# Kernel optimization log

Hardware: AMD Instinct MI355X
Metric: run time of the kernel (lower is better)

The kernel has to match this reference:

```python
import jax, jax.numpy as jnp
import numpy as np

B, N, VDIM = 64, 256, 2048
LRDIM, EMBED = 64, 1024


def setup_inputs() -> dict:
    key = jax.random.key(0)
    ks = jax.random.split(key, 12)
    s = 1.0 / np.sqrt(VDIM)
    return {
        "Vmat": jax.random.normal(ks[0], (B, N, VDIM), dtype=jnp.float32),
        # weight-normed linear_U1: W = g * v / ||v||_row, bias b
        "U1_v": jax.random.normal(ks[1], (LRDIM, VDIM), dtype=jnp.float32) * s,
        "U1_g": jax.random.uniform(ks[2], (LRDIM,), dtype=jnp.float32, minval=0.5, maxval=1.5),
        "U1_b": jax.random.normal(ks[3], (LRDIM,), dtype=jnp.float32) * s,
        "U2_v": jax.random.normal(ks[4], (LRDIM, VDIM), dtype=jnp.float32) * s,
        "U2_g": jax.random.uniform(ks[5], (LRDIM,), dtype=jnp.float32, minval=0.5, maxval=1.5),
        "U2_b": jax.random.normal(ks[6], (LRDIM,), dtype=jnp.float32) * s,
        # final projection + BatchNorm1d affine params
        "W_lin": jax.random.normal(ks[7], (EMBED, VDIM), dtype=jnp.float32) * s,
        "b_lin": jax.random.normal(ks[8], (EMBED,), dtype=jnp.float32) * s,
        "bn_gamma": jnp.ones((EMBED,), dtype=jnp.float32),
        "bn_beta": jnp.zeros((EMBED,), dtype=jnp.float32),
    }


def _weight_norm(v, g):
    # torch weight_norm with dim=0: per output row
    return v * (g / jnp.linalg.norm(v, axis=1))[:, None]


def reference(Vmat, U1_v, U1_g, U1_b, U2_v, U2_g, U2_b, W_lin, b_lin, bn_gamma, bn_beta):
    # forward(Vmat, t_method='uncorr', model_num=6) -> UnCorrVmat_Detail path
    W1 = _weight_norm(U1_v, U1_g)
    W2 = _weight_norm(U2_v, U2_g)
    right = jax.nn.relu(jnp.einsum('bnv,kv->bnk', Vmat, W1) + U1_b)   # [B,N,LR]
    left = jax.nn.relu(jnp.einsum('bnv,kv->bnk', Vmat, W2) + U2_b)    # [B,N,LR]
    uncorr = jnp.einsum('bnk,bmk->bnm', left, right)                   # [B,N,N]
    # vectorized per-batch diag rsqrt normalization
    d = jax.lax.rsqrt(jnp.einsum('bii->bi', uncorr) + 1e-6)            # [B,N]
    uncorr = d[:, None, :] * uncorr * d[:, :, None]
    uncorr = 1.0 + jnp.eye(Vmat.shape[1], dtype=Vmat.dtype) - uncorr
    feats = jnp.mean(jnp.einsum('bnm,bmv->bnv', uncorr, Vmat), axis=1)  # [B,VDIM]
    # linear + BatchNorm1d (training mode: biased batch stats)
    x = feats @ W_lin.T + b_lin                                        # [B,EMBED]
    mu = jnp.mean(x, axis=0)
    var = jnp.mean(jnp.square(x - mu), axis=0)
    return bn_gamma * (x - mu) * jax.lax.rsqrt(var + 1e-5) + bn_beta
```

## Files before the change

kernel.cpp:

```cpp
#include <hip/hip_runtime.h>

#define B_ 64
#define N_ 256
#define V_ 2048
#define E_ 1024
#define MROWS 16384

typedef __bf16 bf16_t;
typedef bf16_t bf16x8 __attribute__((ext_vector_type(8)));
typedef float f32x4 __attribute__((ext_vector_type(4)));

#define OFF_S   0
#define OFF_LR  16384
#define OFF_FT  2113536
#define FTSZ    131072
#define OFF_WB  2637824

__device__ __forceinline__ void gload_lds16(const bf16_t* g, bf16_t* l) {
    __builtin_amdgcn_global_load_lds((const __attribute__((address_space(1))) void*)g,
                                     (__attribute__((address_space(3))) void*)l, 16, 0, 0);
}

__global__ void kprep(const float* __restrict__ U1v, const float* __restrict__ U1g,
                      const float* __restrict__ U2v, const float* __restrict__ U2g,
                      bf16_t* __restrict__ Wb) {
    __shared__ float red[256];
    __shared__ float sc;
    const int r = blockIdx.x;
    const float* v = (r < 64) ? (U1v + (size_t)r * V_) : (U2v + (size_t)(r - 64) * V_);
    float ss = 0.f;
    for (int i = threadIdx.x; i < V_; i += 256) { float x = v[i]; ss += x * x; }
    red[threadIdx.x] = ss;
    __syncthreads();
    for (int o = 128; o > 0; o >>= 1) {
        if (threadIdx.x < (unsigned)o) red[threadIdx.x] += red[threadIdx.x + o];
        __syncthreads();
    }
    if (threadIdx.x == 0) {
        float g = (r < 64) ? U1g[r] : U2g[r - 64];
        sc = g * rsqrtf(red[0]);
    }
    __syncthreads();
    const float s = sc;
    const int k = threadIdx.x * 8;
    float4 f0 = *(const float4*)(v + k);
    float4 f1 = *(const float4*)(v + k + 4);
    bf16x8 o;
    o[0] = (bf16_t)(f0.x * s); o[1] = (bf16_t)(f0.y * s);
    o[2] = (bf16_t)(f0.z * s); o[3] = (bf16_t)(f0.w * s);
    o[4] = (bf16_t)(f1.x * s); o[5] = (bf16_t)(f1.y * s);
    o[6] = (bf16_t)(f1.z * s); o[7] = (bf16_t)(f1.w * s);
    *(bf16x8*)(Wb + (size_t)r * V_ + k) = o;
}

#define BK 128
__global__ __launch_bounds__(256) void gemm_lr(
    const float* __restrict__ V, const bf16_t* __restrict__ Wb,
    const float* __restrict__ U1b, const float* __restrict__ U2b,
    float* __restrict__ LR) {
    __shared__ bf16_t As[32 * BK];
    __shared__ bf16_t Bs[128 * BK];
    const int t = threadIdx.x;
    const int m0 = blockIdx.x * 32;
    const int wv = t >> 6, lane = t & 63;
    const int lm = lane & 15, lq = lane >> 4;
    const int n0w = wv * 32;

    const int ar = t >> 3, au = t & 7;
    const float* aptr = V + (size_t)(m0 + ar) * V_ + au * 8;
    bf16_t* adst0 = &As[ar * BK + ((au ^ (ar & 15)) * 8)];
    bf16_t* adst1 = &As[ar * BK + (((au + 8) ^ (ar & 15)) * 8)];

    const int rloc = lane >> 4, cc = lane & 15;
    const int r15 = wv * 4 + rloc;
    const bf16_t* bgsrc = Wb + (size_t)r15 * V_ + (cc ^ r15) * 8;

    f32x4 acc[2][2];
#pragma unroll
    for (int i = 0; i < 2; ++i)
#pragma unroll
        for (int j = 0; j < 2; ++j) acc[i][j] = (f32x4){0.f, 0.f, 0.f, 0.f};

#pragma unroll
    for (int q = 0; q < 8; ++q)
        gload_lds16(bgsrc + (size_t)q * 16 * V_, &Bs[(q * 16 + wv * 4) * BK]);
    float4 ap0 = *(const float4*)(aptr);
    float4 ap1 = *(const float4*)(aptr + 4);
    float4 ap2 = *(const float4*)(aptr + 64);
    float4 ap3 = *(const float4*)(aptr + 68);

    for (int k0 = 0; k0 < V_; k0 += BK) {
        bf16x8 av0, av1;
        av0[0] = (bf16_t)ap0.x; av0[1] = (bf16_t)ap0.y; av0[2] = (bf16_t)ap0.z; av0[3] = (bf16_t)ap0.w;
        av0[4] = (bf16_t)ap1.x; av0[5] = (bf16_t)ap1.y; av0[6] = (bf16_t)ap1.z; av0[7] = (bf16_t)ap1.w;
        av1[0] = (bf16_t)ap2.x; av1[1] = (bf16_t)ap2.y; av1[2] = (bf16_t)ap2.z; av1[3] = (bf16_t)ap2.w;
        av1[4] = (bf16_t)ap3.x; av1[5] = (bf16_t)ap3.y; av1[6] = (bf16_t)ap3.z; av1[7] = (bf16_t)ap3.w;
        *(bf16x8*)adst0 = av0;
        *(bf16x8*)adst1 = av1;
        __syncthreads();

#pragma unroll
        for (int h = 0; h < 2; ++h) {
            bf16x8 af[2][2], bfr[2][2];
#pragma unroll
            for (int i = 0; i < 2; ++i)
#pragma unroll
                for (int kf = 0; kf < 2; ++kf)
                    af[i][kf] = *(bf16x8*)&As[(i * 16 + lm) * BK + ((((h * 2 + kf) * 4 + lq) ^ lm) * 8)];
#pragma unroll
            for (int j = 0; j < 2; ++j)
#pragma unroll
                for (int kf = 0; kf < 2; ++kf)
                    bfr[j][kf] = *(bf16x8*)&Bs[(n0w + j * 16 + lm) * BK + ((((h * 2 + kf) * 4 + lq) ^ lm) * 8)];
            if (h == 1 && k0 + BK < V_) {
                ap0 = *(const float4*)(aptr + k0 + BK);
                ap1 = *(const float4*)(aptr + k0 + BK + 4);
                ap2 = *(const float4*)(aptr + k0 + BK + 64);
                ap3 = *(const float4*)(aptr + k0 + BK + 68);
            }
#pragma unroll
            for (int i = 0; i < 2; ++i)
#pragma unroll
                for (int j = 0; j < 2; ++j) {
                    acc[i][j] = __builtin_amdgcn_mfma_f32_16x16x32_bf16(af[i][0], bfr[j][0], acc[i][j], 0, 0, 0);
                    acc[i][j] = __builtin_amdgcn_mfma_f32_16x16x32_bf16(af[i][1], bfr[j][1], acc[i][j], 0, 0, 0);
                }
        }
        __syncthreads();
        if (k0 + BK < V_) {
#pragma unroll
            for (int q = 0; q < 8; ++q)
                gload_lds16(bgsrc + (size_t)q * 16 * V_ + (k0 + BK), &Bs[(q * 16 + wv * 4) * BK]);
        }
    }
#pragma unroll
    for (int j = 0; j < 2; ++j) {
        const int n = n0w + j * 16 + lm;
        const float bi = (n < 64) ? U1b[n] : U2b[n - 64];
#pragma unroll
        for (int i = 0; i < 2; ++i)
#pragma unroll
            for (int r = 0; r < 4; ++r) {
                const int m = m0 + i * 16 + lq * 4 + r;
                LR[(size_t)m * 128 + n] = fmaxf(acc[i][j][r] + bi, 0.f);
            }
    }
}

__global__ __launch_bounds__(256) void kds(const float* __restrict__ LR, float* __restrict__ s) {
    __shared__ float dl[256];
    __shared__ float red[4][64];
    __shared__ float lbar[64];
    const int b = blockIdx.x, t = threadIdx.x;
    const float* Lb = LR + (size_t)b * N_ * 128;
    const float* row = Lb + (size_t)t * 128;
    float dd = 0.f;
#pragma unroll
    for (int k = 0; k < 64; k += 4) {
        float4 l = *(const float4*)(row + k);
        float4 r = *(const float4*)(row + 64 + k);
        dd += l.x * r.x + l.y * r.y + l.z * r.z + l.w * r.w;
    }
    const float dv = rsqrtf(dd + 1e-6f);
    dl[t] = dv;
    __syncthreads();
    const int k = t & 63, g = t >> 6;
    float acc = 0.f;
    for (int n = g; n < N_; n += 4)
        acc += dl[n] * Lb[(size_t)n * 128 + 64 + k];
    red[g][k] = acc;
    __syncthreads();
    if (t < 64) lbar[t] = red[0][t] + red[1][t] + red[2][t] + red[3][t];
    __syncthreads();
    float a2 = 0.f;
#pragma unroll 8
    for (int kk = 0; kk < 64; ++kk) a2 += lbar[kk] * row[kk];
    s[b * N_ + t] = ((float)(N_ + 1) - dv * a2) * (1.0f / (float)N_);
}

__global__ __launch_bounds__(256) void kfeats(const float* __restrict__ Vmat,
                                              const float* __restrict__ s,
                                              float* __restrict__ ftp) {
    const int b = blockIdx.x >> 3, vc = (blockIdx.x >> 2) & 1, mc = blockIdx.x & 3;
    __shared__ float sl[64];
    const int t = threadIdx.x;
    if (t < 64) sl[t] = s[b * N_ + mc * 64 + t];
    __syncthreads();
    const int v = vc * 1024 + t * 4;
    const float* base = Vmat + (size_t)b * N_ * V_ + (size_t)mc * 64 * V_ + v;
    float4 a = {0.f, 0.f, 0.f, 0.f};
    for (int m = 0; m < 64; m += 16) {
        float4 x[16];
#pragma unroll
        for (int u = 0; u < 16; ++u) x[u] = *(const float4*)(base + (size_t)(m + u) * V_);
#pragma unroll
        for (int u = 0; u < 16; ++u) {
            float sv = sl[m + u];
            a.x += sv * x[u].x; a.y += sv * x[u].y;
            a.z += sv * x[u].z; a.w += sv * x[u].w;
        }
    }
    float* dst = ftp + (size_t)mc * FTSZ;
    dst[(size_t)(v + 0) * 64 + b] = a.x;
    dst[(size_t)(v + 1) * 64 + b] = a.y;
    dst[(size_t)(v + 2) * 64 + b] = a.z;
    dst[(size_t)(v + 3) * 64 + b] = a.w;
}

__global__ __launch_bounds__(512) void klinbn(const float* __restrict__ ftp,
                                              const float* __restrict__ Wl,
                                              const float* __restrict__ gamma,
                                              const float* __restrict__ beta,
                                              float* __restrict__ out) {
    __shared__ float red[8][4][64];
    const int e0 = blockIdx.x * 4;
    const int t = threadIdx.x, b = t & 63, g = t >> 6;
    const float* w0 = Wl + (size_t)(e0 + 0) * V_ + g * 256;
    const float* w1 = Wl + (size_t)(e0 + 1) * V_ + g * 256;
    const float* w2 = Wl + (size_t)(e0 + 2) * V_ + g * 256;
    const float* w3 = Wl + (size_t)(e0 + 3) * V_ + g * 256;
    const float* f0 = ftp + 0 * FTSZ + (size_t)g * 256 * 64 + b;
    const float* f1 = ftp + 1 * FTSZ + (size_t)g * 256 * 64 + b;
    const float* f2 = ftp + 2 * FTSZ + (size_t)g * 256 * 64 + b;
    const float* f3 = ftp + 3 * FTSZ + (size_t)g * 256 * 64 + b;
    float a0 = 0.f, a1 = 0.f, a2 = 0.f, a3 = 0.f;
#pragma unroll 4
    for (int k = 0; k < 256; ++k) {
        const size_t o = (size_t)k * 64;
        float fv = (f0[o] + f1[o]) + (f2[o] + f3[o]);
        a0 += fv * w0[k]; a1 += fv * w1[k]; a2 += fv * w2[k]; a3 += fv * w3[k];
    }
    red[g][0][b] = a0; red[g][1][b] = a1; red[g][2][b] = a2; red[g][3][b] = a3;
    __syncthreads();
    if (t < 256) {
        const int e = t >> 6;
        float v = 0.f;
#pragma unroll
        for (int gg = 0; gg < 8; ++gg) v += red[gg][e][b];
        float sum = v;
#pragma unroll
        for (int o = 1; o < 64; o <<= 1) sum += __shfl_xor(sum, o, 64);
        float mu = sum * (1.f / 64.f);
        float dvv = v - mu;
        float q = dvv * dvv;
#pragma unroll
        for (int o = 1; o < 64; o <<= 1) q += __shfl_xor(q, o, 64);
        float inv = rsqrtf(q * (1.f / 64.f) + 1e-5f);
        red[0][e][b] = gamma[e0 + e] * dvv * inv + beta[e0 + e];
    }
    __syncthreads();
    if (t < 256) {
        const int b2 = t >> 2, j = t & 3;
        out[(size_t)b2 * E_ + e0 + j] = red[0][j][b2];
    }
}

extern "C" void kernel_launch(void* const* d_in, const int* in_sizes, int n_in,
                              void* d_out, int out_size, void* d_ws, size_t ws_size,
                              hipStream_t stream) {
    const float* Vmat = (const float*)d_in[0];
    const float* U1v  = (const float*)d_in[1];
    const float* U1g  = (const float*)d_in[2];
    const float* U1b  = (const float*)d_in[3];
    const float* U2v  = (const float*)d_in[4];
    const float* U2g  = (const float*)d_in[5];
    const float* U2b  = (const float*)d_in[6];
    const float* Wl   = (const float*)d_in[7];
    const float* gam  = (const float*)d_in[9];
    const float* bet  = (const float*)d_in[10];

    float*  ws     = (float*)d_ws;
    float*  s      = ws + OFF_S;
    float*  LR     = ws + OFF_LR;
    float*  ftp    = ws + OFF_FT;
    bf16_t* Wb     = (bf16_t*)(ws + OFF_WB);

    kprep  <<<128, 256, 0, stream>>>(U1v, U1g, U2v, U2g, Wb);
    gemm_lr<<<MROWS / 32, 256, 0, stream>>>(Vmat, Wb, U1b, U2b, LR);
    kds    <<<B_, 256, 0, stream>>>(LR, s);
    kfeats <<<B_ * 8, 256, 0, stream>>>(Vmat, s, ftp);
    klinbn <<<E_ / 4, 512, 0, stream>>>(ftp, Wl, gam, bet, (float*)d_out);
}
```

Baseline: 289.3 us.

## Double-buffer LDS tiles in low-rank GEMM to overlap loads with MFMA

Doubles the A and B shared-memory tiles in gemm_lr so the next K-slice of both V (fp32 to bf16 converted) and the bf16 weights is fetched into the alternate buffer while MFMAs run on the current one. This drops one of the two barriers per iteration and moves the weight global-to-LDS loads off the critical path. In exchange LDS use doubles to 80 KB per block, which may cut occupancy, and the A prefetch registers now stay live across the whole compute phase.

```diff
diff --git a/kernel.cpp b/kernel.cpp
--- a/kernel.cpp
+++ b/kernel.cpp
@@ -54,12 +54,14 @@
 }
 
 #define BK 128
+#define ASZ (32 * BK)
+#define BSZ (128 * BK)
 __global__ __launch_bounds__(256) void gemm_lr(
     const float* __restrict__ V, const bf16_t* __restrict__ Wb,
     const float* __restrict__ U1b, const float* __restrict__ U2b,
     float* __restrict__ LR) {
-    __shared__ bf16_t As[32 * BK];
-    __shared__ bf16_t Bs[128 * BK];
+    __shared__ bf16_t As[2 * ASZ];
+    __shared__ bf16_t Bs[2 * BSZ];
     const int t = threadIdx.x;
     const int m0 = blockIdx.x * 32;
     const int wv = t >> 6, lane = t & 63;
@@ -68,12 +70,13 @@
 
     const int ar = t >> 3, au = t & 7;
     const float* aptr = V + (size_t)(m0 + ar) * V_ + au * 8;
-    bf16_t* adst0 = &As[ar * BK + ((au ^ (ar & 15)) * 8)];
-    bf16_t* adst1 = &As[ar * BK + (((au + 8) ^ (ar & 15)) * 8)];
+    const int aoff0 = ar * BK + ((au ^ (ar & 15)) * 8);
+    const int aoff1 = ar * BK + (((au + 8) ^ (ar & 15)) * 8);
 
     const int rloc = lane >> 4, cc = lane & 15;
     const int r15 = wv * 4 + rloc;
     const bf16_t* bgsrc = Wb + (size_t)r15 * V_ + (cc ^ r15) * 8;
+    const int bofw = wv * 4 * BK;
 
     f32x4 acc[2][2];
 #pragma unroll
@@ -81,24 +84,39 @@
 #pragma unroll
         for (int j = 0; j < 2; ++j) acc[i][j] = (f32x4){0.f, 0.f, 0.f, 0.f};
 
-#pragma unroll
-    for (int q = 0; q < 8; ++q)
-        gload_lds16(bgsrc + (size_t)q * 16 * V_, &Bs[(q * 16 + wv * 4) * BK]);
     float4 ap0 = *(const float4*)(aptr);
     float4 ap1 = *(const float4*)(aptr + 4);
     float4 ap2 = *(const float4*)(aptr + 64);
     float4 ap3 = *(const float4*)(aptr + 68);
-
-    for (int k0 = 0; k0 < V_; k0 += BK) {
+#pragma unroll
+    for (int q = 0; q < 8; ++q)
+        gload_lds16(bgsrc + (size_t)q * 16 * V_, &Bs[bofw + q * 16 * BK]);
+    {
         bf16x8 av0, av1;
         av0[0] = (bf16_t)ap0.x; av0[1] = (bf16_t)ap0.y; av0[2] = (bf16_t)ap0.z; av0[3] = (bf16_t)ap0.w;
         av0[4] = (bf16_t)ap1.x; av0[5] = (bf16_t)ap1.y; av0[6] = (bf16_t)ap1.z; av0[7] = (bf16_t)ap1.w;
         av1[0] = (bf16_t)ap2.x; av1[1] = (bf16_t)ap2.y; av1[2] = (bf16_t)ap2.z; av1[3] = (bf16_t)ap2.w;
         av1[4] = (bf16_t)ap3.x; av1[5] = (bf16_t)ap3.y; av1[6] = (bf16_t)ap3.z; av1[7] = (bf16_t)ap3.w;
-        *(bf16x8*)adst0 = av0;
-        *(bf16x8*)adst1 = av1;
-        __syncthreads();
-
+        *(bf16x8*)&As[aoff0] = av0;
+        *(bf16x8*)&As[aoff1] = av1;
+    }
+    __syncthreads();
+
+    for (int k0 = 0; k0 < V_; k0 += BK) {
+        const int p = (k0 >> 7) & 1, np = p ^ 1;
+        const bool next = (k0 + BK) < V_;
+        if (next) {
+            ap0 = *(const float4*)(aptr + k0 + BK);
+            ap1 = *(const float4*)(aptr + k0 + BK + 4);
+            ap2 = *(const float4*)(aptr + k0 + BK + 64);
+            ap3 = *(const float4*)(aptr + k0 + BK + 68);
+#pragma unroll
+            for (int q = 0; q < 8; ++q)
+                gload_lds16(bgsrc + (size_t)q * 16 * V_ + (k0 + BK),
+                            &Bs[np * BSZ + bofw + q * 16 * BK]);
+        }
+        const bf16_t* Asp = As + p * ASZ;
+        const bf16_t* Bsp = Bs + p * BSZ;
 #pragma unroll
         for (int h = 0; h < 2; ++h) {
             bf16x8 af[2][2], bfr[2][2];
@@ -106,18 +124,12 @@
             for (int i = 0; i < 2; ++i)
 #pragma unroll
                 for (int kf = 0; kf < 2; ++kf)
-                    af[i][kf] = *(bf16x8*)&As[(i * 16 + lm) * BK + ((((h * 2 + kf) * 4 + lq) ^ lm) * 8)];
+                    af[i][kf] = *(bf16x8*)&Asp[(i * 16 + lm) * BK + ((((h * 2 + kf) * 4 + lq) ^ lm) * 8)];
 #pragma unroll
             for (int j = 0; j < 2; ++j)
 #pragma unroll
                 for (int kf = 0; kf < 2; ++kf)
-                    bfr[j][kf] = *(bf16x8*)&Bs[(n0w + j * 16 + lm) * BK + ((((h * 2 + kf) * 4 + lq) ^ lm) * 8)];
-            if (h == 1 && k0 + BK < V_) {
-                ap0 = *(const float4*)(aptr + k0 + BK);
-                ap1 = *(const float4*)(aptr + k0 + BK + 4);
-                ap2 = *(const float4*)(aptr + k0 + BK + 64);
-                ap3 = *(const float4*)(aptr + k0 + BK + 68);
-            }
+                    bfr[j][kf] = *(bf16x8*)&Bsp[(n0w + j * 16 + lm) * BK + ((((h * 2 + kf) * 4 + lq) ^ lm) * 8)];
 #pragma unroll
             for (int i = 0; i < 2; ++i)
 #pragma unroll
@@ -126,12 +138,16 @@
                     acc[i][j] = __builtin_amdgcn_mfma_f32_16x16x32_bf16(af[i][1], bfr[j][1], acc[i][j], 0, 0, 0);
                 }
         }
+        if (next) {
+            bf16x8 av0, av1;
+            av0[0] = (bf16_t)ap0.x; av0[1] = (bf16_t)ap0.y; av0[2] = (bf16_t)ap0.z; av0[3] = (bf16_t)ap0.w;
+            av0[4] = (bf16_t)ap1.x; av0[5] = (bf16_t)ap1.y; av0[6] = (bf16_t)ap1.z; av0[7] = (bf16_t)ap1.w;
+            av1[0] = (bf16_t)ap2.x; av1[1] = (bf16_t)ap2.y; av1[2] = (bf16_t)ap2.z; av1[3] = (bf16_t)ap2.w;
+            av1[4] = (bf16_t)ap3.x; av1[5] = (bf16_t)ap3.y; av1[6] = (bf16_t)ap3.z; av1[7] = (bf16_t)ap3.w;
+            *(bf16x8*)&As[np * ASZ + aoff0] = av0;
+            *(bf16x8*)&As[np * ASZ + aoff1] = av1;
+        }
         __syncthreads();
-        if (k0 + BK < V_) {
-#pragma unroll
-            for (int q = 0; q < 8; ++q)
-                gload_lds16(bgsrc + (size_t)q * 16 * V_ + (k0 + BK), &Bs[(q * 16 + wv * 4) * BK]);
-        }
     }
 #pragma unroll
     for (int j = 0; j < 2; ++j) {
```

Result: slower. 298.3 us (+3.1%).
